# Kernel tuning notes

Hardware: AMD Instinct MI355X
Metric: run time of the kernel (lower is better)

## Reference

```python
import jax, jax.numpy as jnp
import numpy as np

VOCAB = 30000
FEAT = 30000
HID = 1024
EMB = 1024
B, LQ, LKV = 32, 256, 256


def setup_inputs() -> dict:
    key = jax.random.key(0)
    ks = jax.random.split(key, 8)
    captions = jax.random.randint(ks[0], (B, LKV), 0, VOCAB)
    targets_feature = jax.random.randint(ks[1], (B, LKV), 0, FEAT)
    hidden_state = jax.random.normal(ks[2], (B, LQ, HID), dtype=jnp.float32)
    feature_mask = jax.random.uniform(ks[3], (B, LQ, LKV), dtype=jnp.float32)
    # embeddings initialized uniform(-0.1, 0.1) per init_weights
    Wa = jax.random.uniform(ks[4], (VOCAB, HID), minval=-0.1, maxval=0.1, dtype=jnp.float32)
    Wc = jax.random.uniform(ks[5], (FEAT, HID), minval=-0.1, maxval=0.1, dtype=jnp.float32)
    r = np.sqrt(6.0) / np.sqrt(2 * HID + EMB)
    fc_w = jax.random.uniform(ks[6], (EMB, 2 * HID), minval=-r, maxval=r, dtype=jnp.float32)
    fc_b = jnp.zeros((EMB,), dtype=jnp.float32)
    return {"captions": captions, "hidden_state": hidden_state,
            "targets_feature": targets_feature, "feature_mask": feature_mask,
            "Wa": Wa, "Wc": Wc, "fc_w": fc_w, "fc_b": fc_b}


def reference(captions, hidden_state, targets_feature, feature_mask, Wa, Wc, fc_w, fc_b):
    ea = Wa[captions]           # [B, LKV, H]
    ec = Wc[targets_feature]    # [B, LKV, H]
    # u = hidden_state @ embedding_a^T : [B, LQ, LKV]
    u = jnp.einsum('bqh,bkh->bqk', hidden_state, ea)
    mask = jnp.clip(feature_mask, 0.0, 1.0)
    delta = jnp.exp(u) * mask
    p = delta / (jnp.sum(delta, axis=2, keepdims=True) + 1e-10)  # masked softmax-like weights
    # weighted value sum without materializing [B,LQ,LKV,H] broadcasts
    o = jnp.einsum('bqk,bkh->bqh', p, ec)
    o = jnp.concatenate([hidden_state, o], axis=2)               # [B, LQ, 2H]
    o = o @ fc_w.T + fc_b                                        # [B, LQ, EMB]
    o = o + 1e-10
    norm = jnp.sqrt(jnp.sum(o * o, axis=-1, keepdims=True)) + 1e-8
    return o / norm
```

## Files before the change

### kernel.cpp

```cpp
#include <hip/hip_runtime.h>
#include <hip/hip_bf16.h>

typedef __attribute__((ext_vector_type(8))) short short8;
typedef __attribute__((ext_vector_type(4))) float f32x4;
using bf16 = __hip_bfloat16;


#define VMCNT(n) asm volatile("s_waitcnt vmcnt(" #n ")" ::: "memory")
#define LGK0     asm volatile("s_waitcnt lgkmcnt(0)" ::: "memory")
#define SBAR     __builtin_amdgcn_sched_barrier(0)

__device__ __forceinline__ void glds16(const void* g, void* lds) {
  __builtin_amdgcn_global_load_lds(
      (const __attribute__((address_space(1))) void*)g,
      (__attribute__((address_space(3))) void*)lds, 16, 0, 0);
}

__device__ __forceinline__ void barrier_raw() {
  asm volatile("" ::: "memory");
  __builtin_amdgcn_s_barrier();
  asm volatile("" ::: "memory");
}

__global__ __launch_bounds__(256) void k1_prep(
    const int* __restrict__ captions, const float* __restrict__ Wa,
    const float* __restrict__ H, const float* __restrict__ fcw,
    const int* __restrict__ targets, const float* __restrict__ Wc,
    bf16* __restrict__ EA, bf16* __restrict__ X, bf16* __restrict__ FW,
    bf16* __restrict__ ECT) {
  __shared__ float T[64][67];
  int task = blockIdx.x;
  int tid = threadIdx.x;
  if (task < 17408) {
    const float* src;
    bf16* dst;
    int n;
    if (task < 8192) {
      src = Wa + (size_t)captions[task] * 1024;
      dst = EA + (size_t)task * 1024;
      n = 1024;
    } else if (task < 16384) {
      int t = task - 8192;
      src = H + (size_t)t * 1024;
      dst = X + (size_t)t * 2048;
      n = 1024;
    } else {
      int t = task - 16384;
      src = fcw + (size_t)t * 2048;
      dst = FW + (size_t)t * 2048;
      n = 2048;
    }
    for (int c = tid * 4; c < n; c += 1024) {
      float4 v = *(const float4*)(src + c);
      __hip_bfloat162 p0, p1;
      p0.x = __float2bfloat16(v.x); p0.y = __float2bfloat16(v.y);
      p1.x = __float2bfloat16(v.z); p1.y = __float2bfloat16(v.w);
      *(__hip_bfloat162*)(dst + c) = p0;
      *(__hip_bfloat162*)(dst + c + 2) = p1;
    }
    return;
  }
  int bid = task - 17408;
  int b = bid >> 6;
  int kt = (bid >> 4) & 3;
  int ht = bid & 15;
#pragma unroll
  for (int p = 0; p < 4; ++p) {
    int k = p * 16 + (tid >> 4);
    int idx = targets[b * 256 + kt * 64 + k];
    const float* s = Wc + (size_t)idx * 1024 + ht * 64 + (tid & 15) * 4;
    float4 v = *(const float4*)s;
    int c = (tid & 15) * 4;
    T[k][c] = v.x; T[k][c + 1] = v.y; T[k][c + 2] = v.z; T[k][c + 3] = v.w;
  }
  __syncthreads();
#pragma unroll
  for (int p = 0; p < 8; ++p) {
    int h = p * 8 + (tid >> 5);
    int k = (tid & 31) * 2;
    __hip_bfloat162 o;
    o.x = __float2bfloat16(T[k][h]);
    o.y = __float2bfloat16(T[k + 1][h]);
    *(__hip_bfloat162*)(ECT + ((size_t)b * 1024 + ht * 64 + h) * 256 + kt * 64 + k) = o;
  }
}

__global__ __launch_bounds__(256, 1) void k23_scores_pv(
    bf16* __restrict__ X, const bf16* __restrict__ EA,
    const bf16* __restrict__ ECT, const float* __restrict__ mask) {
  __shared__ __align__(16) char smem[16 * 1024 + 512 + 128 * 1024];
  bf16* p_lds = (bf16*)smem;
  float* red  = (float*)(smem + 16 * 1024);
  bf16* big   = (bf16*)(smem + 16 * 1024 + 512);

  int p = blockIdx.x;
  int wg = (p & 7) * 32 + (p >> 3);
  int b = wg >> 3;
  int mb = wg & 7;
  int tid = threadIdx.x, w = tid >> 6, l = tid & 63;

  const bf16* Ag = X + ((size_t)b * 256 + mb * 32) * 2048;
  const bf16* Bg = EA + (size_t)b * 256 * 1024;
  bf16* As = big;
  bf16* Bs = big + 32 * 64;

  f32x4 sacc[2][4];
  f32x4 zero = {0.f, 0.f, 0.f, 0.f};
#pragma unroll
  for (int m2 = 0; m2 < 2; ++m2)
#pragma unroll
    for (int n = 0; n < 4; ++n) sacc[m2][n] = zero;

  for (int kt = 0; kt < 16; ++kt) {
    {
      int row = tid >> 3, ss = (tid & 7) ^ (row & 7);
      glds16(Ag + (size_t)row * 2048 + kt * 64 + ss * 8,
             As + (size_t)w * 64 * 8);
    }
#pragma unroll
    for (int i = 0; i < 8; ++i) {
      int c = i * 256 + tid;
      int row = c >> 3, ss = (c & 7) ^ (row & 7);
      glds16(Bg + (size_t)row * 1024 + kt * 64 + ss * 8,
             Bs + (size_t)(i * 256 + w * 64) * 8);
    }
    __syncthreads();
#pragma unroll
    for (int kk = 0; kk < 2; ++kk) {
      short8 a2[2];
#pragma unroll
      for (int m2 = 0; m2 < 2; ++m2) {
        int ar = m2 * 16 + (l & 15);
        int sl = kk * 4 + (l >> 4);
        a2[m2] = *(const short8*)(As + ar * 64 + ((sl ^ (ar & 7)) * 8));
      }
      __builtin_amdgcn_s_setprio(1);
#pragma unroll
      for (int n = 0; n < 4; ++n) {
        int rb = w * 64 + n * 16 + (l & 15);
        int sl = kk * 4 + (l >> 4);
        short8 bfr = *(const short8*)(Bs + rb * 64 + ((sl ^ (rb & 7)) * 8));
#pragma unroll
        for (int m2 = 0; m2 < 2; ++m2)
          sacc[m2][n] = __builtin_amdgcn_mfma_f32_16x16x32_bf16(
              a2[m2], bfr, sacc[m2][n], 0, 0, 0);
      }
      __builtin_amdgcn_s_setprio(0);
    }
    __syncthreads();
  }

  const float* mrow = mask + ((size_t)b * 256 + mb * 32) * 256;
  float s[2][4] = {{0.f, 0.f, 0.f, 0.f}, {0.f, 0.f, 0.f, 0.f}};
#pragma unroll
  for (int m2 = 0; m2 < 2; ++m2)
#pragma unroll
    for (int n = 0; n < 4; ++n)
#pragma unroll
      for (int i = 0; i < 4; ++i) {
        int r = m2 * 16 + ((l >> 4) << 2) + i;
        int c = w * 64 + n * 16 + (l & 15);
        float mv = mrow[r * 256 + c];
        mv = fminf(fmaxf(mv, 0.f), 1.f);
        float ev = expf(sacc[m2][n][i]) * mv;
        sacc[m2][n][i] = ev;
        s[m2][i] += ev;
      }
#pragma unroll
  for (int msk = 1; msk < 16; msk <<= 1)
#pragma unroll
    for (int m2 = 0; m2 < 2; ++m2)
#pragma unroll
      for (int i = 0; i < 4; ++i) s[m2][i] += __shfl_xor(s[m2][i], msk, 64);
  if ((l & 15) == 0) {
#pragma unroll
    for (int m2 = 0; m2 < 2; ++m2)
#pragma unroll
      for (int i = 0; i < 4; ++i)
        red[w * 32 + m2 * 16 + ((l >> 4) << 2) + i] = s[m2][i];
  }
  __syncthreads();
  float inv[2][4];
#pragma unroll
  for (int m2 = 0; m2 < 2; ++m2)
#pragma unroll
    for (int i = 0; i < 4; ++i) {
      int r = m2 * 16 + ((l >> 4) << 2) + i;
      float tot = red[r] + red[32 + r] + red[64 + r] + red[96 + r];
      inv[m2][i] = 1.f / (tot + 1e-10f);
    }
#pragma unroll
  for (int m2 = 0; m2 < 2; ++m2)
#pragma unroll
    for (int n = 0; n < 4; ++n)
#pragma unroll
      for (int i = 0; i < 4; ++i) {
        int r = m2 * 16 + ((l >> 4) << 2) + i;
        int c = w * 64 + n * 16 + (l & 15);
        float pv = sacc[m2][n][i] * inv[m2][i];
        p_lds[r * 256 + (((c >> 3) ^ (r & 7)) << 3) + (c & 7)] =
            __float2bfloat16(pv);
      }
  __syncthreads();

  bf16* XO = X + ((size_t)b * 256 + mb * 32) * 2048 + 1024;
  for (int np = 0; np < 2; ++np) {
    f32x4 acc[2][8];
#pragma unroll
    for (int m2 = 0; m2 < 2; ++m2)
#pragma unroll
      for (int n = 0; n < 8; ++n) acc[m2][n] = zero;

#pragma unroll
    for (int it = 0; it < 16; ++it) {
      int g = it * 64 + l;
      int row = g >> 3, ss = (g & 7) ^ (row & 7);
      glds16(ECT + ((size_t)b * 1024 + np * 512 + w * 128 + row) * 256 + ss * 8,
             big + (size_t)(0 * 4 + w) * 8192 + (size_t)it * 512);
    }
    __syncthreads();
    for (int kt = 0; kt < 4; ++kt) {
      int cur = kt & 1;
      if (kt < 3) {
#pragma unroll
        for (int it = 0; it < 16; ++it) {
          int g = it * 64 + l;
          int row = g >> 3, ss = (g & 7) ^ (row & 7);
          glds16(ECT + ((size_t)b * 1024 + np * 512 + w * 128 + row) * 256 +
                     (kt + 1) * 64 + ss * 8,
                 big + (size_t)((cur ^ 1) * 4 + w) * 8192 + (size_t)it * 512);
        }
      }
      const bf16* Bw = big + (size_t)(cur * 4 + w) * 8192;
#pragma unroll
      for (int kk = 0; kk < 2; ++kk) {
        short8 a2[2];
#pragma unroll
        for (int m2 = 0; m2 < 2; ++m2) {
          int ar = m2 * 16 + (l & 15);
          int sl = kt * 8 + kk * 4 + (l >> 4);
          a2[m2] = *(const short8*)(p_lds + ar * 256 + ((sl ^ (ar & 7)) * 8));
        }
        __builtin_amdgcn_s_setprio(1);
#pragma unroll
        for (int n = 0; n < 8; ++n) {
          int rb = n * 16 + (l & 15);
          int sl = kk * 4 + (l >> 4);
          short8 bfr = *(const short8*)(Bw + rb * 64 + ((sl ^ (rb & 7)) * 8));
#pragma unroll
          for (int m2 = 0; m2 < 2; ++m2)
            acc[m2][n] = __builtin_amdgcn_mfma_f32_16x16x32_bf16(
                a2[m2], bfr, acc[m2][n], 0, 0, 0);
        }
        __builtin_amdgcn_s_setprio(0);
      }
      __syncthreads();
    }
#pragma unroll
    for (int m2 = 0; m2 < 2; ++m2)
#pragma unroll
      for (int n = 0; n < 8; ++n) {
        int rl = m2 * 16 + ((l >> 4) << 2);
        int col = np * 512 + w * 128 + n * 16 + (l & 15);
#pragma unroll
        for (int i = 0; i < 4; ++i)
          XO[(size_t)(rl + i) * 2048 + col] = __float2bfloat16(acc[m2][n][i]);
      }
  }
}

#define K4E (256 * 64 + 128 * 64)

__device__ __forceinline__ void k4_stage(const bf16* __restrict__ Ag,
                                         const bf16* __restrict__ Bg, int kt,
                                         bf16* Lb, int tid, int w) {
#pragma unroll
  for (int i = 0; i < 4; ++i) {
    int c = i * 512 + tid;
    int row = c >> 3, ss = (c & 7) ^ (row & 7);
    glds16(Ag + (size_t)row * 2048 + kt * 64 + ss * 8,
           Lb + (size_t)(i * 512 + w * 64) * 8);
  }
#pragma unroll
  for (int i = 0; i < 2; ++i) {
    int c = i * 512 + tid;
    int row = c >> 3, ss = (c & 7) ^ (row & 7);
    glds16(Bg + (size_t)row * 2048 + kt * 64 + ss * 8,
           Lb + (size_t)(256 * 64 + (i * 512 + w * 64) * 8));
  }
}

__device__ __forceinline__ void k4_tile(const bf16* Lb, int wr, int wc, int l,
                                        f32x4 (&acc)[4][4]) {
  const bf16* As = Lb;
  const bf16* Bs = Lb + 256 * 64;
  short8 a[2][4], b[2][4];
#pragma unroll
  for (int kk = 0; kk < 2; ++kk)
#pragma unroll
    for (int n = 0; n < 4; ++n) {
      int row = wc * 64 + n * 16 + (l & 15);
      int slot = kk * 4 + (l >> 4);
      b[kk][n] = *(const short8*)(Bs + row * 64 + ((slot ^ (row & 7)) * 8));
    }
#pragma unroll
  for (int kk = 0; kk < 2; ++kk)
#pragma unroll
    for (int m = 0; m < 4; ++m) {
      int row = wr * 64 + m * 16 + (l & 15);
      int slot = kk * 4 + (l >> 4);
      a[kk][m] = *(const short8*)(As + row * 64 + ((slot ^ (row & 7)) * 8));
    }
  __builtin_amdgcn_s_setprio(1);
#pragma unroll
  for (int kk = 0; kk < 2; ++kk)
#pragma unroll
    for (int m = 0; m < 4; ++m)
#pragma unroll
      for (int n = 0; n < 4; ++n)
        acc[m][n] = __builtin_amdgcn_mfma_f32_16x16x32_bf16(
            a[kk][m], b[kk][n], acc[m][n], 0, 0, 0);
  __builtin_amdgcn_s_setprio(0);
}

__global__ __launch_bounds__(512, 1) void k4_fc(
    const bf16* __restrict__ X, const bf16* __restrict__ FW,
    const float* __restrict__ fcb, float* __restrict__ out) {
  __shared__ __align__(16) bf16 L[3][K4E];
  int p = blockIdx.x;
  int wg = (p & 7) * 32 + (p >> 3);
  int mb = wg >> 3;
  int nb = wg & 7;
  int tid = threadIdx.x, w = tid >> 6, l = tid & 63;
  int wr = w >> 1, wc = w & 1;
  f32x4 acc[4][4];
  f32x4 zero = {0.f, 0.f, 0.f, 0.f};
#pragma unroll
  for (int m = 0; m < 4; ++m)
#pragma unroll
    for (int n = 0; n < 4; ++n) acc[m][n] = zero;

  const bf16* Ag = X + (size_t)mb * 256 * 2048;
  const bf16* Bg = FW + (size_t)nb * 128 * 2048;

  k4_stage(Ag, Bg, 0, L[0], tid, w);
  k4_stage(Ag, Bg, 1, L[1], tid, w);

#define K4_BODY(T, C, S)                                   \
  k4_stage(Ag, Bg, (T) + 2, L[S], tid, w);                 \
  VMCNT(12); SBAR;                                         \
  barrier_raw(); SBAR;                                     \
  k4_tile(L[C], wr, wc, l, acc);                           \
  LGK0; SBAR;                                              \
  barrier_raw();

  for (int tt = 0; tt < 30; tt += 3) {
    K4_BODY(tt + 0, 0, 2)
    K4_BODY(tt + 1, 1, 0)
    K4_BODY(tt + 2, 2, 1)
  }
#undef K4_BODY
  VMCNT(6); SBAR;
  barrier_raw(); SBAR;
  k4_tile(L[0], wr, wc, l, acc);
  LGK0; SBAR;
  barrier_raw();
  VMCNT(0); SBAR;
  barrier_raw(); SBAR;
  k4_tile(L[1], wr, wc, l, acc);

  float bias[4];
#pragma unroll
  for (int n = 0; n < 4; ++n)
    bias[n] = fcb[nb * 128 + wc * 64 + n * 16 + (l & 15)];
#pragma unroll
  for (int m = 0; m < 4; ++m) {
    int rbase = mb * 256 + wr * 64 + m * 16 + ((l >> 4) << 2);
#pragma unroll
    for (int n = 0; n < 4; ++n) {
      int col = nb * 128 + wc * 64 + n * 16 + (l & 15);
#pragma unroll
      for (int i = 0; i < 4; ++i)
        out[(size_t)(rbase + i) * 1024 + col] = acc[m][n][i] + bias[n] + 1e-10f;
    }
  }
}

__global__ __launch_bounds__(256) void k5_norm(float* __restrict__ y) {
  __shared__ float red[4];
  int row = blockIdx.x;
  float* p = y + (size_t)row * 1024;
  int tid = threadIdx.x;
  float4 v = *(const float4*)(p + tid * 4);
  float ss = v.x * v.x + v.y * v.y + v.z * v.z + v.w * v.w;
#pragma unroll
  for (int m = 1; m < 64; m <<= 1) ss += __shfl_xor(ss, m, 64);
  if ((tid & 63) == 0) red[tid >> 6] = ss;
  __syncthreads();
  float tot = red[0] + red[1] + red[2] + red[3];
  float inv = 1.f / (sqrtf(tot) + 1e-8f);
  float4 o;
  o.x = v.x * inv; o.y = v.y * inv; o.z = v.z * inv; o.w = v.w * inv;
  *(float4*)(p + tid * 4) = o;
}

extern "C" void kernel_launch(void* const* d_in, const int* in_sizes, int n_in,
                              void* d_out, int out_size, void* d_ws, size_t ws_size,
                              hipStream_t stream) {
  const int* captions = (const int*)d_in[0];
  const float* H = (const float*)d_in[1];
  const int* targets = (const int*)d_in[2];
  const float* mask = (const float*)d_in[3];
  const float* Wa = (const float*)d_in[4];
  const float* Wc = (const float*)d_in[5];
  const float* fcw = (const float*)d_in[6];
  const float* fcb = (const float*)d_in[7];
  float* out = (float*)d_out;

  char* ws = (char*)d_ws;
  bf16* EA = (bf16*)(ws);
  bf16* ECT = (bf16*)(ws + (16u << 20));
  bf16* X = (bf16*)(ws + (36u << 20));
  bf16* FW = (bf16*)(ws + (68u << 20));

  k1_prep<<<19456, 256, 0, stream>>>(captions, Wa, H, fcw, targets, Wc,
                                     EA, X, FW, ECT);
  k23_scores_pv<<<256, 256, 0, stream>>>(X, EA, ECT, mask);
  k4_fc<<<256, 512, 0, stream>>>(X, FW, fcb, out);
  k5_norm<<<8192, 256, 0, stream>>>(out);
}
```

Baseline: 109.7 us.

## Triple-buffer the scores GEMM K-loop with async global-to-LDS prefetch

```diff
diff --git a/kernel.cpp b/kernel.cpp
--- a/kernel.cpp
+++ b/kernel.cpp
@@ -85,6 +85,51 @@
   }
 }
 
+__device__ __forceinline__ void k23_sstage(const bf16* __restrict__ Ag,
+                                           const bf16* __restrict__ Bg, int kt,
+                                           bf16* buf, int tid, int w) {
+  {
+    int row = tid >> 3, ss = (tid & 7) ^ (row & 7);
+    glds16(Ag + (size_t)row * 2048 + kt * 64 + ss * 8,
+           buf + (size_t)w * 64 * 8);
+  }
+#pragma unroll
+  for (int i = 0; i < 8; ++i) {
+    int c = i * 256 + tid;
+    int row = c >> 3, ss = (c & 7) ^ (row & 7);
+    glds16(Bg + (size_t)row * 1024 + kt * 64 + ss * 8,
+           buf + 2048 + (size_t)(i * 256 + w * 64) * 8);
+  }
+}
+
+__device__ __forceinline__ void k23_stile(const bf16* buf, int w, int l,
+                                          f32x4 (&sacc)[2][4]) {
+  const bf16* As = buf;
+  const bf16* Bs = buf + 2048;
+#pragma unroll
+  for (int kk = 0; kk < 2; ++kk) {
+    short8 a2[2];
+#pragma unroll
+    for (int m2 = 0; m2 < 2; ++m2) {
+      int ar = m2 * 16 + (l & 15);
+      int sl = kk * 4 + (l >> 4);
+      a2[m2] = *(const short8*)(As + ar * 64 + ((sl ^ (ar & 7)) * 8));
+    }
+    __builtin_amdgcn_s_setprio(1);
+#pragma unroll
+    for (int n = 0; n < 4; ++n) {
+      int rb = w * 64 + n * 16 + (l & 15);
+      int sl = kk * 4 + (l >> 4);
+      short8 bfr = *(const short8*)(Bs + rb * 64 + ((sl ^ (rb & 7)) * 8));
+#pragma unroll
+      for (int m2 = 0; m2 < 2; ++m2)
+        sacc[m2][n] = __builtin_amdgcn_mfma_f32_16x16x32_bf16(
+            a2[m2], bfr, sacc[m2][n], 0, 0, 0);
+    }
+    __builtin_amdgcn_s_setprio(0);
+  }
+}
+
 __global__ __launch_bounds__(256, 1) void k23_scores_pv(
     bf16* __restrict__ X, const bf16* __restrict__ EA,
     const bf16* __restrict__ ECT, const float* __restrict__ mask) {
@@ -101,8 +146,9 @@
 
   const bf16* Ag = X + ((size_t)b * 256 + mb * 32) * 2048;
   const bf16* Bg = EA + (size_t)b * 256 * 1024;
-  bf16* As = big;
-  bf16* Bs = big + 32 * 64;
+  bf16* S0 = big;
+  bf16* S1 = big + 18432;
+  bf16* S2 = big + 36864;
 
   f32x4 sacc[2][4];
   f32x4 zero = {0.f, 0.f, 0.f, 0.f};
@@ -111,44 +157,33 @@
 #pragma unroll
     for (int n = 0; n < 4; ++n) sacc[m2][n] = zero;
 
-  for (int kt = 0; kt < 16; ++kt) {
-    {
-      int row = tid >> 3, ss = (tid & 7) ^ (row & 7);
-      glds16(Ag + (size_t)row * 2048 + kt * 64 + ss * 8,
-             As + (size_t)w * 64 * 8);
-    }
-#pragma unroll
-    for (int i = 0; i < 8; ++i) {
-      int c = i * 256 + tid;
-      int row = c >> 3, ss = (c & 7) ^ (row & 7);
-      glds16(Bg + (size_t)row * 1024 + kt * 64 + ss * 8,
-             Bs + (size_t)(i * 256 + w * 64) * 8);
-    }
-    __syncthreads();
-#pragma unroll
-    for (int kk = 0; kk < 2; ++kk) {
-      short8 a2[2];
-#pragma unroll
-      for (int m2 = 0; m2 < 2; ++m2) {
-        int ar = m2 * 16 + (l & 15);
-        int sl = kk * 4 + (l >> 4);
-        a2[m2] = *(const short8*)(As + ar * 64 + ((sl ^ (ar & 7)) * 8));
-      }
-      __builtin_amdgcn_s_setprio(1);
-#pragma unroll
-      for (int n = 0; n < 4; ++n) {
-        int rb = w * 64 + n * 16 + (l & 15);
-        int sl = kk * 4 + (l >> 4);
-        short8 bfr = *(const short8*)(Bs + rb * 64 + ((sl ^ (rb & 7)) * 8));
-#pragma unroll
-        for (int m2 = 0; m2 < 2; ++m2)
-          sacc[m2][n] = __builtin_amdgcn_mfma_f32_16x16x32_bf16(
-              a2[m2], bfr, sacc[m2][n], 0, 0, 0);
-      }
-      __builtin_amdgcn_s_setprio(0);
-    }
-    __syncthreads();
-  }
+  k23_sstage(Ag, Bg, 0, S0, tid, w);
+  k23_sstage(Ag, Bg, 1, S1, tid, w);
+
+#define SBODY(T, C, S)                                \
+  k23_sstage(Ag, Bg, (T) + 2, S, tid, w);             \
+  VMCNT(18); SBAR;                                    \
+  barrier_raw(); SBAR;                                \
+  k23_stile(C, w, l, sacc);                           \
+  LGK0; SBAR;                                         \
+  barrier_raw();
+
+  for (int tt = 0; tt < 12; tt += 3) {
+    SBODY(tt + 0, S0, S2)
+    SBODY(tt + 1, S1, S0)
+    SBODY(tt + 2, S2, S1)
+  }
+  SBODY(12, S0, S2)
+  SBODY(13, S1, S0)
+#undef SBODY
+  VMCNT(9); SBAR;
+  barrier_raw(); SBAR;
+  k23_stile(S2, w, l, sacc);
+  LGK0; SBAR;
+  barrier_raw();
+  VMCNT(0); SBAR;
+  barrier_raw(); SBAR;
+  k23_stile(S0, w, l, sacc);
 
   const float* mrow = mask + ((size_t)b * 256 + mb * 32) * 256;
   float s[2][4] = {{0.f, 0.f, 0.f, 0.f}, {0.f, 0.f, 0.f, 0.f}};
```

New measurement: 104.2 us. 1.05x faster.
